# Kernel tuning notes

Hardware: AMD Instinct MI355X
Metric: run time of the kernel (lower is better)

Reference implementation:

```python
import jax, jax.numpy as jnp
import numpy as np

B, L, F, H, O = 128, 2048, 128, 256, 128
NT = 5  # tickersteps


def setup_inputs() -> dict:
    key = jax.random.key(0)
    ks = jax.random.split(key, 10)
    x = jax.random.normal(ks[0], (B, L, F), dtype=jnp.float32)
    true_seq_lens = jax.random.randint(ks[1], (B,), 1, L + 1)
    s = 0.05
    W = jax.random.normal(ks[2], (F, 3 * H), dtype=jnp.float32) * s   # fwd weights [ci|ig|og]
    R = jax.random.normal(ks[3], (H, 3 * H), dtype=jnp.float32) * s   # recurrent weights [ci|ig|og]
    # biases: b_ci=0, b_ig ~ N(-5,1), b_og=0  (forget gate has no weights/bias -> fg = 1)
    b_ig = jax.random.normal(ks[4], (H,), dtype=jnp.float32) - 5.0
    b = jnp.concatenate([jnp.zeros(H, jnp.float32), b_ig, jnp.zeros(H, jnp.float32)])
    b_ticker = jax.random.normal(ks[5], (3 * H,), dtype=jnp.float32) * s  # tickerstep biases
    Wp = jax.random.normal(ks[6], (H, H), dtype=jnp.float32) * s
    bp = jnp.zeros((H,), jnp.float32)
    Wo = jax.random.normal(ks[7], (O, H), dtype=jnp.float32) * s
    bo = jnp.zeros((O,), jnp.float32)
    return {"x": x, "true_seq_lens": true_seq_lens, "W": W, "R": R, "b": b,
            "b_ticker": b_ticker, "Wp": Wp, "bp": bp, "Wo": Wo, "bo": bo}


def _lstm_final_h(x, true_seq_lens, W, R, b, b_ticker):
    Bv, Lv, _ = x.shape
    Hv = R.shape[0]
    T = Lv + NT
    xp = jnp.pad(x, ((0, 0), (0, NT), (0, 0)))            # zero input during tickersteps
    xs = jnp.swapaxes(xp, 0, 1)                            # [T, B, F]
    ts = jnp.arange(T)
    lens = true_seq_lens.astype(jnp.int32)

    def step(carry, inp):
        h, c = carry
        x_t, t = inp
        in_seq = t < lens                                  # [B]
        in_tick = (t >= lens) & (t < lens + NT)
        active = in_seq | in_tick
        x_t = jnp.where(in_seq[:, None], x_t, 0.0)
        pre = x_t @ W + h @ R + b + jnp.where(in_tick[:, None], b_ticker, 0.0)  # [B, 3H]
        ci = jnp.tanh(pre[:, :Hv])
        ig = jax.nn.sigmoid(pre[:, Hv:2 * Hv])
        og = jax.nn.sigmoid(pre[:, 2 * Hv:])
        c_new = c + ci * ig                                # forget gate disabled -> fg = 1
        h_new = jnp.tanh(c_new) * og
        m = active[:, None]
        return (jnp.where(m, h_new, h), jnp.where(m, c_new, c)), None

    h0 = jnp.zeros((Bv, Hv), x.dtype)
    c0 = jnp.zeros((Bv, Hv), x.dtype)
    (h, _), _ = jax.lax.scan(step, (h0, c0), (xs, ts))
    return h


def reference(x, true_seq_lens, W, R, b, b_ticker, Wp, bp, Wo, bo):
    h = _lstm_final_h(x, true_seq_lens, W, R, b, b_ticker)   # [B, H] final state after tickersteps
    h = h @ Wp.T + bp                                        # pre_fc_out
    return h @ Wo.T + bo                                     # fc_out
```

## Files before the change

### kernel.cpp

```cpp
#include <hip/hip_runtime.h>

#define BB    128
#define LL    2048
#define FF    128
#define HH    256
#define OO    128
#define NTICK 5
#define GC    16
#define NCG   8
#define CH    4
#define DRING 128
#define NPS   8
#define NPL   16
#define MAXT  (LL + NTICK)
#define MAXCH ((MAXT + CH - 1) / CH)
#define RDY8  0x0101010101010101ULL

#define SC_CI  (2.8853900817779268f)
#define SC_GT  (-1.4426950408889634f)

typedef __attribute__((ext_vector_type(8))) _Float16 half8;
typedef __attribute__((ext_vector_type(2))) __fp16 fp16x2;
typedef __attribute__((ext_vector_type(4))) float f32x4;

union U64H4 { unsigned long long u; _Float16 h[4]; fp16x2 p[2]; };

__device__ __forceinline__ float fast_rcp(float x) { return __builtin_amdgcn_rcpf(x); }
__device__ __forceinline__ float fast_exp2(float x) { return __builtin_amdgcn_exp2f(x); }

__device__ __forceinline__ unsigned long long sysload_u64(const unsigned long long* p) {
  return __hip_atomic_load(p, __ATOMIC_RELAXED, __HIP_MEMORY_SCOPE_SYSTEM);
}
__device__ __forceinline__ void sysstore_u64(unsigned long long* p, unsigned long long v) {
  __hip_atomic_store(p, v, __ATOMIC_RELAXED, __HIP_MEMORY_SCOPE_SYSTEM);
}
__device__ __forceinline__ int sysload_i32(const int* p) {
  return __hip_atomic_load(p, __ATOMIC_RELAXED, __HIP_MEMORY_SCOPE_SYSTEM);
}
__device__ __forceinline__ void sysstore_i32(int* p, int v) {
  __hip_atomic_store(p, v, __ATOMIC_RELAXED, __HIP_MEMORY_SCOPE_SYSTEM);
}
__device__ __forceinline__ void sysstore_u8(unsigned char* p, unsigned char v) {
  __hip_atomic_store(p, v, __ATOMIC_RELAXED, __HIP_MEMORY_SCOPE_SYSTEM);
}

__device__ __forceinline__ void sync_lds_only() {
  asm volatile("s_waitcnt lgkmcnt(0)" ::: "memory");
  __builtin_amdgcn_s_barrier();
  asm volatile("" ::: "memory");
}

extern "C" __global__ __launch_bounds__(512, 1)
void lstm_all(const float* __restrict__ x, const int* __restrict__ lens,
              const float* __restrict__ W, const float* __restrict__ R,
              const float* __restrict__ bvec, const float* __restrict__ btk,
              unsigned long long* ring, unsigned char* readyb,
              int* prog, float* __restrict__ h_final)
{
  const int tid  = threadIdx.x;
  const int lane = tid & 63;
  const int wv   = tid >> 6;
  const int quad = lane >> 4;
  const int nl   = lane & 15;
  const int bx   = blockIdx.x;

  __shared__ int lens_s[BB];
  if (tid < BB) lens_s[tid] = lens[tid];
  __syncthreads();

  if (bx < NCG) {
    const int cg = bx, cbase = cg * GC;
    __shared__ float    pre_s[GC][772];
    __shared__ _Float16 h_s[GC][264];

    for (int i = tid; i < GC * 772; i += 512) ((float*)pre_s)[i] = 0.f;
    for (int i = tid; i < GC * 264; i += 512) ((_Float16*)h_s)[i] = (_Float16)0.f;

    int mxl = 0;
    #pragma unroll
    for (int i = 0; i < GC; i++) mxl = max(mxl, lens_s[cbase + i]);
    const int Tg = mxl + NTICK;

    half8 rfr[6][8];
    const int colw = wv * 96;
    #pragma unroll
    for (int tile = 0; tile < 6; tile++) {
      const int scol = colw + tile * 16;
      const float rsc = (scol < HH) ? SC_CI : SC_GT;
      const int col = scol + nl;
      #pragma unroll
      for (int kc = 0; kc < 8; kc++) {
        const int k0 = kc * 32 + quad * 8;
        half8 v;
        #pragma unroll
        for (int j = 0; j < 8; j++) v[j] = (_Float16)(R[(k0 + j) * (3 * HH) + col] * rsc);
        rfr[tile][kc] = v;
      }
    }

    const int m   = tid >> 5;
    const int q32 = tid & 31;
    const int d0  = q32 * 4;
    const int lenm = lens_s[cbase + m];

    float cst[8];
    #pragma unroll
    for (int d = 0; d < 8; d++) cst[d] = 0.f;

    const unsigned long long* rb = (const unsigned long long*)readyb;

    while (sysload_u64(rb + 0) != RDY8) {}
    asm volatile("" ::: "memory");
    unsigned long long xw[6];
    {
      const unsigned long long* rp = ring + (((long)0 * BB + cbase + m) * 192) + q32;
      xw[0] = sysload_u64(rp);       xw[1] = sysload_u64(rp + 32);
      xw[2] = sysload_u64(rp + 64);  xw[3] = sysload_u64(rp + 96);
      xw[4] = sysload_u64(rp + 128); xw[5] = sysload_u64(rp + 160);
    }
    unsigned long long rvn = sysload_u64(rb + 1);
    int cur_chunk = 0;
    __syncthreads();

    for (int t = 0; t < Tg; ++t) {
      if (t > 0) {
        f32x4 acc[6];
        #pragma unroll
        for (int i = 0; i < 6; i++) acc[i] = (f32x4){0.f, 0.f, 0.f, 0.f};
        const _Float16* hrow = &h_s[nl][0];
        #pragma unroll
        for (int kc = 0; kc < 8; kc++) {
          const half8 a = *(const half8*)(hrow + kc * 32 + quad * 8);
          #pragma unroll
          for (int tile = 0; tile < 6; tile++)
            acc[tile] = __builtin_amdgcn_mfma_f32_16x16x32_f16(rfr[tile][kc], a, acc[tile], 0, 0, 0);
        }
        #pragma unroll
        for (int tile = 0; tile < 6; tile++)
          *(f32x4*)(&pre_s[nl][colw + tile * 16 + quad * 4]) = acc[tile];
      }
      sync_lds_only();

      unsigned long long xwc[6];
      #pragma unroll
      for (int i = 0; i < 6; i++) xwc[i] = xw[i];

      if (t + 1 < Tg && t + 1 < lenm + NTICK) {
        const int nc = (t + 1) >> 2;
        if (nc != cur_chunk) {
          while (rvn != RDY8) rvn = sysload_u64(rb + nc);
          cur_chunk = nc;
          rvn = (nc + 1 < MAXCH) ? sysload_u64(rb + nc + 1) : RDY8;
        }
        asm volatile("" ::: "memory");
        const int slot = (t + 1) & (DRING - 1);
        const unsigned long long* rp = ring + (((long)slot * BB + cbase + m) * 192) + q32;
        xw[0] = sysload_u64(rp);       xw[1] = sysload_u64(rp + 32);
        xw[2] = sysload_u64(rp + 64);  xw[3] = sysload_u64(rp + 96);
        xw[4] = sysload_u64(rp + 128); xw[5] = sysload_u64(rp + 160);
      }

      if (t < lenm + NTICK) {
        const float* pr = &pre_s[m][0];
        #pragma unroll
        for (int k = 0; k < 2; k++) {
          const int dk = d0 + 128 * k;
          U64H4 uck, uik, uok;
          uck.u = xwc[k];
          uik.u = xwc[2 + k];
          uok.u = xwc[4 + k];
          const f32x4 pci4 = *(const f32x4*)(pr + dk);
          const f32x4 pig4 = *(const f32x4*)(pr + 256 + dk);
          const f32x4 pog4 = *(const f32x4*)(pr + 512 + dk);
          float hh[4];
          #pragma unroll
          for (int r = 0; r < 4; r++) {
            const float pc = pci4[r] + (float)uck.h[r];
            const float pi = pig4[r] + (float)uik.h[r];
            const float po = pog4[r] + (float)uok.h[r];
            const float ea = fast_exp2(__builtin_fminf(pc, 43.0f));
            const float eb = fast_exp2(pi);
            const float t1 = __builtin_fmaf(ea, SC_CI, -SC_CI);
            const float cn = __builtin_fmaf(t1, fast_rcp((ea + 1.f) * (1.f + eb)), cst[k * 4 + r]);
            const float ec = fast_exp2(__builtin_fminf(cn, 43.0f));
            const float ed = fast_exp2(po);
            hh[r] = (ec - 1.f) * fast_rcp((ec + 1.f) * (1.f + ed));
            cst[k * 4 + r] = cn;
          }
          U64H4 up;
          up.p[0] = __builtin_amdgcn_cvt_pkrtz(hh[0], hh[1]);
          up.p[1] = __builtin_amdgcn_cvt_pkrtz(hh[2], hh[3]);
          *(unsigned long long*)(&h_s[m][dk]) = up.u;
          if (t == lenm + NTICK - 1) {
            float4 v; v.x = hh[0]; v.y = hh[1]; v.z = hh[2]; v.w = hh[3];
            *(float4*)(h_final + (cbase + m) * HH + dk) = v;
          }
        }
      }

      sync_lds_only();
      if (tid == 0) sysstore_i32(prog + cg, t);
    }
    if (tid == 0) sysstore_i32(prog + cg, 1 << 20);

  } else {
    const int pid = bx - NCG;
    const int s   = pid & 7;
    const int pl  = pid >> 3;

    int mxall = 0;
    #pragma unroll 8
    for (int i = 0; i < BB; i++) mxall = max(mxall, lens_s[i]);
    const int Tall = mxall + NTICK;
    const int nch  = (Tall + CH - 1) / CH;

    half8 wfr[4];
    float bias4[4], tick4[4];
    int col0w = 0;
    if (wv < 6) {
      col0w = s * 96 + wv * 16;
      const float wsc = (col0w < HH) ? SC_CI : SC_GT;
      #pragma unroll
      for (int kc = 0; kc < 4; kc++) {
        const int k0 = kc * 32 + quad * 8;
        half8 v;
        #pragma unroll
        for (int j = 0; j < 8; j++) v[j] = (_Float16)(W[(k0 + j) * (3 * HH) + col0w + nl] * wsc);
        wfr[kc] = v;
      }
      float4 b4 = *(const float4*)(bvec + col0w + quad * 4);
      float4 t4 = *(const float4*)(btk  + col0w + quad * 4);
      bias4[0] = b4.x * wsc; bias4[1] = b4.y * wsc; bias4[2] = b4.z * wsc; bias4[3] = b4.w * wsc;
      tick4[0] = t4.x * wsc; tick4[1] = t4.y * wsc; tick4[2] = t4.z * wsc; tick4[3] = t4.w * wsc;
    }

    for (int c = pl; c < nch; c += NPL) {
      if (c * CH >= DRING) {
        if (tid == 0) {
          const int need = c * CH + CH - DRING;
          for (;;) {
            int mn = 0x7fffffff;
            #pragma unroll
            for (int g = 0; g < NCG; g++) mn = min(mn, sysload_i32(prog + g));
            if (mn >= need) break;
          }
        }
        __syncthreads();
      }
      if (wv < 6) {
        for (int tt = 0; tt < CH; tt++) {
          const int t = c * CH + tt;
          const int slot = t & (DRING - 1);
          #pragma unroll 2
          for (int bt = 0; bt < 8; bt++) {
            const int b = bt * 16 + nl;
            const int lenb = lens_s[b];
            f32x4 acc = {0.f, 0.f, 0.f, 0.f};
            if (t < LL) {
              const float* xp = x + ((long)b * LL + t) * FF + quad * 8;
              #pragma unroll
              for (int kc = 0; kc < 4; kc++) {
                const float4 u0 = *(const float4*)(xp + kc * 32);
                const float4 u1 = *(const float4*)(xp + kc * 32 + 4);
                half8 a;
                a[0] = (_Float16)u0.x; a[1] = (_Float16)u0.y;
                a[2] = (_Float16)u0.z; a[3] = (_Float16)u0.w;
                a[4] = (_Float16)u1.x; a[5] = (_Float16)u1.y;
                a[6] = (_Float16)u1.z; a[7] = (_Float16)u1.w;
                acc = __builtin_amdgcn_mfma_f32_16x16x32_f16(wfr[kc], a, acc, 0, 0, 0);
              }
            }
            U64H4 pk;
            const bool in_x  = (t < lenb);
            const bool in_tk = (t >= lenb) && (t < lenb + NTICK);
            #pragma unroll
            for (int r = 0; r < 4; r++) {
              float v = bias4[r];
              if (in_x)  v += acc[r];
              if (in_tk) v += tick4[r];
              pk.h[r] = (_Float16)v;
            }
            sysstore_u64(ring + ((((long)slot * BB + b) * 768 + col0w + quad * 4) >> 2), pk.u);
          }
        }
      }
      __syncthreads();
      if (tid == 0) sysstore_u8(readyb + c * 8 + s, (unsigned char)1);
    }
  }
}

extern "C" __global__ void proj_hp(const float* __restrict__ h,
                                   const float* __restrict__ Wp,
                                   const float* __restrict__ bp,
                                   float* __restrict__ hp)
{
  const int bb = blockIdx.x;
  const int j  = threadIdx.x;
  const float4* hv = (const float4*)(h + bb * HH);
  const float4* wr = (const float4*)(Wp + j * HH);
  float s = 0.f;
  for (int k = 0; k < HH / 4; k++) {
    const float4 a = hv[k], w = wr[k];
    s += a.x * w.x + a.y * w.y + a.z * w.z + a.w * w.w;
  }
  hp[bb * HH + j] = s + bp[j];
}

extern "C" __global__ void proj_out(const float* __restrict__ hp,
                                    const float* __restrict__ Wo,
                                    const float* __restrict__ bo,
                                    float* __restrict__ out)
{
  const int bb = blockIdx.x;
  const int o  = threadIdx.x;
  const float4* hv = (const float4*)(hp + bb * HH);
  const float4* wr = (const float4*)(Wo + o * HH);
  float s = 0.f;
  for (int k = 0; k < HH / 4; k++) {
    const float4 a = hv[k], w = wr[k];
    s += a.x * w.x + a.y * w.y + a.z * w.z + a.w * w.w;
  }
  out[bb * OO + o] = s + bo[o];
}

extern "C" void kernel_launch(void* const* d_in, const int* in_sizes, int n_in,
                              void* d_out, int out_size, void* d_ws, size_t ws_size,
                              hipStream_t stream)
{
  const float* x    = (const float*)d_in[0];
  const int*   ln   = (const int*)  d_in[1];
  const float* W    = (const float*)d_in[2];
  const float* R    = (const float*)d_in[3];
  const float* bvec = (const float*)d_in[4];
  const float* btk  = (const float*)d_in[5];
  const float* Wp   = (const float*)d_in[6];
  const float* bp   = (const float*)d_in[7];
  const float* Wo   = (const float*)d_in[8];
  const float* bo   = (const float*)d_in[9];
  float* out = (float*)d_out;

  char* ws = (char*)d_ws;
  int*                prog    = (int*)ws;
  unsigned char*      readyb  = (unsigned char*)(ws + 64);
  float*              h_final = (float*)(ws + 8192);
  float*              hp      = (float*)(ws + 8192 + 131072);
  unsigned long long* ring    = (unsigned long long*)(ws + (1 << 20));

  hipLaunchKernelGGL(lstm_all, dim3(NCG + NPS * NPL), dim3(512), 0, stream,
                     x, ln, W, R, bvec, btk, ring, readyb, prog, h_final);
  hipLaunchKernelGGL(proj_hp,  dim3(BB), dim3(HH), 0, stream, h_final, Wp, bp, hp);
  hipLaunchKernelGGL(proj_out, dim3(BB), dim3(OO), 0, stream, hp, Wo, bo, out);
}
```

Measured before the change: 5.882 ms.

## Interleave two batch groups per recurrent block to overlap MFMA with gate math

```diff
diff --git a/kernel.cpp b/kernel.cpp
--- a/kernel.cpp
+++ b/kernel.cpp
@@ -7,7 +7,8 @@
 #define OO    128
 #define NTICK 5
 #define GC    16
-#define NCG   8
+#define NGRP  8
+#define NCG   4
 #define CH    4
 #define DRING 128
 #define NPS   8
@@ -69,17 +70,20 @@
   __syncthreads();
 
   if (bx < NCG) {
-    const int cg = bx, cbase = cg * GC;
-    __shared__ float    pre_s[GC][772];
-    __shared__ _Float16 h_s[GC][264];
-
-    for (int i = tid; i < GC * 772; i += 512) ((float*)pre_s)[i] = 0.f;
-    for (int i = tid; i < GC * 264; i += 512) ((_Float16*)h_s)[i] = (_Float16)0.f;
-
-    int mxl = 0;
+    const int cg = bx, cbase = cg * 32;
+    __shared__ float    preA[GC][772], preB[GC][772];
+    __shared__ _Float16 hA[GC][264],  hB[GC][264];
+
+    for (int i = tid; i < GC * 772; i += 512) { ((float*)preA)[i] = 0.f; ((float*)preB)[i] = 0.f; }
+    for (int i = tid; i < GC * 264; i += 512) { ((_Float16*)hA)[i] = (_Float16)0.f; ((_Float16*)hB)[i] = (_Float16)0.f; }
+
+    int mxA = 0, mxB = 0;
     #pragma unroll
-    for (int i = 0; i < GC; i++) mxl = max(mxl, lens_s[cbase + i]);
-    const int Tg = mxl + NTICK;
+    for (int i = 0; i < GC; i++) {
+      mxA = max(mxA, lens_s[cbase + i]);
+      mxB = max(mxB, lens_s[cbase + 16 + i]);
+    }
+    const int TL = max(mxA + NTICK, mxB + NTICK + 1);
 
     half8 rfr[6][8];
     const int colw = wv * 96;
@@ -101,107 +105,147 @@
     const int m   = tid >> 5;
     const int q32 = tid & 31;
     const int d0  = q32 * 4;
-    const int lenm = lens_s[cbase + m];
-
-    float cst[8];
+    const int lenA = lens_s[cbase + m];
+    const int lenB = lens_s[cbase + 16 + m];
+    const int chainA = cbase + m, chainB = cbase + 16 + m;
+
+    float cstA[8], cstB[8];
     #pragma unroll
-    for (int d = 0; d < 8; d++) cst[d] = 0.f;
+    for (int d = 0; d < 8; d++) { cstA[d] = 0.f; cstB[d] = 0.f; }
 
     const unsigned long long* rb = (const unsigned long long*)readyb;
 
-    while (sysload_u64(rb + 0) != RDY8) {}
-    asm volatile("" ::: "memory");
-    unsigned long long xw[6];
-    {
-      const unsigned long long* rp = ring + (((long)0 * BB + cbase + m) * 192) + q32;
+    auto pf = [&](int time, int chain, unsigned long long* xw, int& cur, unsigned long long& rvn) {
+      const int nc = time >> 2;
+      if (nc != cur) {
+        while (rvn != RDY8) rvn = sysload_u64(rb + nc);
+        cur = nc;
+        rvn = (nc + 1 < MAXCH) ? sysload_u64(rb + nc + 1) : RDY8;
+      }
+      asm volatile("" ::: "memory");
+      const int slot = time & (DRING - 1);
+      const unsigned long long* rp = ring + (((long)slot * BB + chain) * 192) + q32;
       xw[0] = sysload_u64(rp);       xw[1] = sysload_u64(rp + 32);
       xw[2] = sysload_u64(rp + 64);  xw[3] = sysload_u64(rp + 96);
       xw[4] = sysload_u64(rp + 128); xw[5] = sysload_u64(rp + 160);
-    }
-    unsigned long long rvn = sysload_u64(rb + 1);
-    int cur_chunk = 0;
+    };
+
+    auto gate_fn = [&](int s, int lenm, float* cst, float (*pre)[772],
+                       _Float16 (*hsx)[264], const unsigned long long* xc, int chain) {
+      const float* pr = &pre[m][0];
+      #pragma unroll
+      for (int k = 0; k < 2; k++) {
+        const int dk = d0 + 128 * k;
+        U64H4 uck, uik, uok;
+        uck.u = xc[k]; uik.u = xc[2 + k]; uok.u = xc[4 + k];
+        const f32x4 pci4 = *(const f32x4*)(pr + dk);
+        const f32x4 pig4 = *(const f32x4*)(pr + 256 + dk);
+        const f32x4 pog4 = *(const f32x4*)(pr + 512 + dk);
+        float hh[4];
+        #pragma unroll
+        for (int r = 0; r < 4; r++) {
+          const float pc = pci4[r] + (float)uck.h[r];
+          const float pi = pig4[r] + (float)uik.h[r];
+          const float po = pog4[r] + (float)uok.h[r];
+          const float ea = fast_exp2(__builtin_fminf(pc, 43.0f));
+          const float eb = fast_exp2(pi);
+          const float t1 = __builtin_fmaf(ea, SC_CI, -SC_CI);
+          const float cn = __builtin_fmaf(t1, fast_rcp((ea + 1.f) * (1.f + eb)), cst[k * 4 + r]);
+          const float ec = fast_exp2(__builtin_fminf(cn, 43.0f));
+          const float ed = fast_exp2(po);
+          hh[r] = (ec - 1.f) * fast_rcp((ec + 1.f) * (1.f + ed));
+          cst[k * 4 + r] = cn;
+        }
+        U64H4 up;
+        up.p[0] = __builtin_amdgcn_cvt_pkrtz(hh[0], hh[1]);
+        up.p[1] = __builtin_amdgcn_cvt_pkrtz(hh[2], hh[3]);
+        *(unsigned long long*)(&hsx[m][dk]) = up.u;
+        if (s == lenm + NTICK - 1) {
+          float4 v; v.x = hh[0]; v.y = hh[1]; v.z = hh[2]; v.w = hh[3];
+          *(float4*)(h_final + chain * HH + dk) = v;
+        }
+      }
+    };
+
+    while (sysload_u64(rb + 0) != RDY8) {}
+    asm volatile("" ::: "memory");
+    unsigned long long xwA[6], xwB[6] = {0, 0, 0, 0, 0, 0};
+    {
+      const unsigned long long* rp = ring + ((long)chainA * 192) + q32;
+      xwA[0] = sysload_u64(rp);       xwA[1] = sysload_u64(rp + 32);
+      xwA[2] = sysload_u64(rp + 64);  xwA[3] = sysload_u64(rp + 96);
+      xwA[4] = sysload_u64(rp + 128); xwA[5] = sysload_u64(rp + 160);
+    }
+    unsigned long long rvnA = sysload_u64(rb + 1);
+    unsigned long long rvnB = sysload_u64(rb + 1);
+    int curA = 0, curB = 0;
     __syncthreads();
 
-    for (int t = 0; t < Tg; ++t) {
-      if (t > 0) {
+    for (int t = 0; t < TL; ++t) {
+      {
         f32x4 acc[6];
         #pragma unroll
         for (int i = 0; i < 6; i++) acc[i] = (f32x4){0.f, 0.f, 0.f, 0.f};
-        const _Float16* hrow = &h_s[nl][0];
-        #pragma unroll
-        for (int kc = 0; kc < 8; kc++) {
-          const half8 a = *(const half8*)(hrow + kc * 32 + quad * 8);
+        if (t > 0) {
+          const _Float16* hrow = &hA[nl][0];
+          #pragma unroll
+          for (int kc = 0; kc < 8; kc++) {
+            const half8 a = *(const half8*)(hrow + kc * 32 + quad * 8);
+            #pragma unroll
+            for (int tile = 0; tile < 6; tile++)
+              acc[tile] = __builtin_amdgcn_mfma_f32_16x16x32_f16(rfr[tile][kc], a, acc[tile], 0, 0, 0);
+          }
+        }
+        unsigned long long xc[6];
+        #pragma unroll
+        for (int i = 0; i < 6; i++) xc[i] = xwB[i];
+        if (t < lenB + NTICK) pf(t, chainB, xwB, curB, rvnB);
+        if (t >= 1 && t - 1 < lenB + NTICK)
+          gate_fn(t - 1, lenB, cstB, preB, hB, xc, chainB);
+        if (t > 0) {
           #pragma unroll
           for (int tile = 0; tile < 6; tile++)
-            acc[tile] = __builtin_amdgcn_mfma_f32_16x16x32_f16(rfr[tile][kc], a, acc[tile], 0, 0, 0);
-        }
-        #pragma unroll
-        for (int tile = 0; tile < 6; tile++)
-          *(f32x4*)(&pre_s[nl][colw + tile * 16 + quad * 4]) = acc[tile];
+            *(f32x4*)(&preA[nl][colw + tile * 16 + quad * 4]) = acc[tile];
+        }
       }
       sync_lds_only();
 
-      unsigned long long xwc[6];
-      #pragma unroll
-      for (int i = 0; i < 6; i++) xwc[i] = xw[i];
-
-      if (t + 1 < Tg && t + 1 < lenm + NTICK) {
-        const int nc = (t + 1) >> 2;
-        if (nc != cur_chunk) {
-          while (rvn != RDY8) rvn = sysload_u64(rb + nc);
-          cur_chunk = nc;
-          rvn = (nc + 1 < MAXCH) ? sysload_u64(rb + nc + 1) : RDY8;
-        }
-        asm volatile("" ::: "memory");
-        const int slot = (t + 1) & (DRING - 1);
-        const unsigned long long* rp = ring + (((long)slot * BB + cbase + m) * 192) + q32;
-        xw[0] = sysload_u64(rp);       xw[1] = sysload_u64(rp + 32);
-        xw[2] = sysload_u64(rp + 64);  xw[3] = sysload_u64(rp + 96);
-        xw[4] = sysload_u64(rp + 128); xw[5] = sysload_u64(rp + 160);
-      }
-
-      if (t < lenm + NTICK) {
-        const float* pr = &pre_s[m][0];
-        #pragma unroll
-        for (int k = 0; k < 2; k++) {
-          const int dk = d0 + 128 * k;
-          U64H4 uck, uik, uok;
-          uck.u = xwc[k];
-          uik.u = xwc[2 + k];
-          uok.u = xwc[4 + k];
-          const f32x4 pci4 = *(const f32x4*)(pr + dk);
-          const f32x4 pig4 = *(const f32x4*)(pr + 256 + dk);
-          const f32x4 pog4 = *(const f32x4*)(pr + 512 + dk);
-          float hh[4];
+      {
+        f32x4 acc[6];
+        #pragma unroll
+        for (int i = 0; i < 6; i++) acc[i] = (f32x4){0.f, 0.f, 0.f, 0.f};
+        if (t > 0) {
+          const _Float16* hrow = &hB[nl][0];
           #pragma unroll
-          for (int r = 0; r < 4; r++) {
-            const float pc = pci4[r] + (float)uck.h[r];
-            const float pi = pig4[r] + (float)uik.h[r];
-            const float po = pog4[r] + (float)uok.h[r];
-            const float ea = fast_exp2(__builtin_fminf(pc, 43.0f));
-            const float eb = fast_exp2(pi);
-            const float t1 = __builtin_fmaf(ea, SC_CI, -SC_CI);
-            const float cn = __builtin_fmaf(t1, fast_rcp((ea + 1.f) * (1.f + eb)), cst[k * 4 + r]);
-            const float ec = fast_exp2(__builtin_fminf(cn, 43.0f));
-            const float ed = fast_exp2(po);
-            hh[r] = (ec - 1.f) * fast_rcp((ec + 1.f) * (1.f + ed));
-            cst[k * 4 + r] = cn;
+          for (int kc = 0; kc < 8; kc++) {
+            const half8 a = *(const half8*)(hrow + kc * 32 + quad * 8);
+            #pragma unroll
+            for (int tile = 0; tile < 6; tile++)
+              acc[tile] = __builtin_amdgcn_mfma_f32_16x16x32_f16(rfr[tile][kc], a, acc[tile], 0, 0, 0);
           }
-          U64H4 up;
-          up.p[0] = __builtin_amdgcn_cvt_pkrtz(hh[0], hh[1]);
-          up.p[1] = __builtin_amdgcn_cvt_pkrtz(hh[2], hh[3]);
-          *(unsigned long long*)(&h_s[m][dk]) = up.u;
-          if (t == lenm + NTICK - 1) {
-            float4 v; v.x = hh[0]; v.y = hh[1]; v.z = hh[2]; v.w = hh[3];
-            *(float4*)(h_final + (cbase + m) * HH + dk) = v;
-          }
-        }
-      }
-
+        }
+        unsigned long long xc[6];
+        #pragma unroll
+        for (int i = 0; i < 6; i++) xc[i] = xwA[i];
+        if (t + 1 < lenA + NTICK) pf(t + 1, chainA, xwA, curA, rvnA);
+        if (t < lenA + NTICK)
+          gate_fn(t, lenA, cstA, preA, hA, xc, chainA);
+        if (t > 0) {
+          #pragma unroll
+          for (int tile = 0; tile < 6; tile++)
+            *(f32x4*)(&preB[nl][colw + tile * 16 + quad * 4]) = acc[tile];
+        }
+      }
       sync_lds_only();
-      if (tid == 0) sysstore_i32(prog + cg, t);
-    }
-    if (tid == 0) sysstore_i32(prog + cg, 1 << 20);
+      if (tid == 0) {
+        sysstore_i32(prog + 2 * cg, t);
+        sysstore_i32(prog + 2 * cg + 1, t - 1);
+      }
+    }
+    if (tid == 0) {
+      sysstore_i32(prog + 2 * cg, 1 << 20);
+      sysstore_i32(prog + 2 * cg + 1, 1 << 20);
+    }
 
   } else {
     const int pid = bx - NCG;
@@ -241,7 +285,7 @@
           for (;;) {
             int mn = 0x7fffffff;
             #pragma unroll
-            for (int g = 0; g < NCG; g++) mn = min(mn, sysload_i32(prog + g));
+            for (int g = 0; g < NGRP; g++) mn = min(mn, sysload_i32(prog + g));
             if (mn >= need) break;
           }
         }
```

Measured after the change: 21.37 ms. 263% more time.
